# Optimization experiments

Hardware: AMD Instinct MI355X
Metric: run time of the kernel (lower is better)

## Reference

```python
import jax, jax.numpy as jnp
import numpy as np
import math

B, S, E, H, DK, DV = 2, 2048, 1024, 16, 64, 64
EPS = 1e-06


def setup_inputs() -> dict:
    key = jax.random.key(0)
    ks = jax.random.split(key, 11)
    s_in = 1.0 / math.sqrt(E)
    return {
        "query": jax.random.normal(ks[0], (B, S, E), jnp.float32),
        "key_in": jax.random.normal(ks[1], (B, S, E), jnp.float32),
        "value_in": jax.random.normal(ks[2], (B, S, E), jnp.float32),
        "residual_x": jax.random.normal(ks[3], (B, S, E), jnp.float32),
        # stacked per-head Linear params (torch Linear: y = x @ W.T + b); here W stored as [H, E, d]
        "Wq": jax.random.uniform(ks[4], (H, E, DK), jnp.float32, -s_in, s_in),
        "bq": jax.random.uniform(ks[5], (H, DK), jnp.float32, -s_in, s_in),
        "Wk": jax.random.uniform(ks[6], (H, E, DK), jnp.float32, -s_in, s_in),
        "bk": jax.random.uniform(ks[7], (H, DK), jnp.float32, -s_in, s_in),
        "Wv": jax.random.uniform(ks[8], (H, E, DV), jnp.float32, -s_in, s_in),
        "bv": jax.random.uniform(ks[9], (H, DV), jnp.float32, -s_in, s_in),
        "ln_scale": jnp.ones((E,), jnp.float32),
        "ln_shift": jnp.zeros((E,), jnp.float32),
    }


def reference(query, key_in, value_in, residual_x, Wq, bq, Wk, bk, Wv, bv, ln_scale, ln_shift):
    # batched per-head projections (replaces python loop over heads)
    q = jnp.einsum("bse,hed->bhsd", query, Wq) + bq[None, :, None, :]
    k = jnp.einsum("bse,hed->bhsd", key_in, Wk) + bk[None, :, None, :]
    v = jnp.einsum("bse,hed->bhsd", value_in, Wv) + bv[None, :, None, :]
    scores = jnp.einsum("bhsd,bhtd->bhst", q, k) / math.sqrt(DK)  # [B,H,S,S]
    causal = jnp.tril(jnp.ones((S, S), bool))  # mask strictly-upper triangle to -inf
    scores = jnp.where(causal[None, None], scores, -jnp.inf)
    attn = jax.nn.softmax(scores, axis=-1)
    out = jnp.einsum("bhst,bhtd->bhsd", attn, v)
    # concat heads along feature dim (head order = cat order)
    out = out.transpose(0, 2, 1, 3).reshape(B, S, H * DV)
    x = out + residual_x
    # custom LayerNorm: unbiased std, shift added into denominator
    mean = x.mean(-1, keepdims=True)
    std = jnp.sqrt(jnp.sum((x - mean) ** 2, axis=-1, keepdims=True) / (E - 1))
    div = std + EPS + ln_shift  # broadcasts [B,S,1]+[E] -> [B,S,E]
    return ln_scale * (x - mean) / div
```

## Files before the change

### kernel.cpp

```cpp
#include <hip/hip_runtime.h>
#include <hip/hip_bf16.h>

#define NB 2
#define NS 2048
#define NE 1024
#define NH 16
#define ND 64
#define MTOT (NB * NS)

typedef __attribute__((ext_vector_type(8))) short bf8_t;
typedef __attribute__((ext_vector_type(4))) short bf4_t;
typedef __attribute__((ext_vector_type(4))) float f32x4;

__device__ __forceinline__ short f2bf(float f) {
    union { float f; unsigned u; } v; v.f = f;
    return (short)((v.u + 0x7FFFu + ((v.u >> 16) & 1u)) >> 16);
}

#define GLOAD16(g, l) __builtin_amdgcn_global_load_lds( \
    (const __attribute__((address_space(1))) void*)(g), \
    (__attribute__((address_space(3))) void*)(l), 16, 0, 0)

__global__ __launch_bounds__(256) void conv_kernel(
    const float* __restrict__ src, short* __restrict__ out)
{
    const size_t nchunk = (size_t)MTOT * NE / 8;
    const size_t stride = (size_t)gridDim.x * 256;
    for (size_t i = (size_t)blockIdx.x * 256 + threadIdx.x; i < nchunk; i += stride) {
        size_t e = i * 8;
        float4 x0 = *(const float4*)(src + e);
        float4 x1 = *(const float4*)(src + e + 4);
        bf8_t o;
        o[0] = f2bf(x0.x); o[1] = f2bf(x0.y); o[2] = f2bf(x0.z); o[3] = f2bf(x0.w);
        o[4] = f2bf(x1.x); o[5] = f2bf(x1.y); o[6] = f2bf(x1.z); o[7] = f2bf(x1.w);
        *(bf8_t*)(out + e) = o;
    }
}

__global__ __launch_bounds__(256) void wt_kernel(
    const float* __restrict__ Wq, const float* __restrict__ Wk, const float* __restrict__ Wv,
    short* __restrict__ wt)
{
    const int p = blockIdx.x / NH, h = blockIdx.x % NH;
    const int e0 = blockIdx.y * 64;
    const float* W = (p == 0) ? Wq : (p == 1) ? Wk : Wv;
    const int t = threadIdx.x;
    const int er = t >> 2, dc = (t & 3) * 16;
    const float* src = W + ((size_t)h * NE + e0 + er) * ND + dc;
    short* dst = wt + (size_t)(p * NH + h) * ND * NE;
#pragma unroll
    for (int j = 0; j < 16; j += 4) {
        float4 x = *(const float4*)(src + j);
        dst[(size_t)(dc + j + 0) * NE + e0 + er] = f2bf(x.x);
        dst[(size_t)(dc + j + 1) * NE + e0 + er] = f2bf(x.y);
        dst[(size_t)(dc + j + 2) * NE + e0 + er] = f2bf(x.z);
        dst[(size_t)(dc + j + 3) * NE + e0 + er] = f2bf(x.w);
    }
}

__global__ __launch_bounds__(256) void proj_kernel(
    const short* __restrict__ A, const short* __restrict__ Bm,
    const float* __restrict__ bias_all, int p, short* __restrict__ outp)
{
    __shared__ __attribute__((aligned(16))) short As[128 * 32];
    __shared__ __attribute__((aligned(16))) short Bs[128 * 32];

    const int m0 = blockIdx.x * 128, n0 = blockIdx.y * 128;
    const int t = threadIdx.x, lane = t & 63, w = t >> 6;
    const int l15 = lane & 15, g = lane >> 4;
    const int wr = w >> 1, wc = w & 1;

    const int srow = t >> 2, scol = (t & 3) * 8;
    const short* ag = A + (size_t)(m0 + srow) * NE + scol;
    const short* bg = Bm + (size_t)(n0 + srow) * NE + scol;
    short* asl = As + t * 8;
    short* bsl = Bs + t * 8;

    f32x4 acc[4][4];
#pragma unroll
    for (int i = 0; i < 4; ++i)
#pragma unroll
        for (int j = 0; j < 4; ++j) acc[i][j] = (f32x4){0.f, 0.f, 0.f, 0.f};

    for (int k0 = 0; k0 < NE; k0 += 32) {
        __syncthreads();
        GLOAD16(ag + k0, asl);
        GLOAD16(ag + k0 + (size_t)64 * NE, asl + 2048);
        GLOAD16(bg + k0, bsl);
        GLOAD16(bg + k0 + (size_t)64 * NE, bsl + 2048);
        __syncthreads();
        bf8_t af[4], bfr[4];
#pragma unroll
        for (int mf = 0; mf < 4; ++mf)
            af[mf] = *(const bf8_t*)&As[(wr * 64 + mf * 16 + l15) * 32 + g * 8];
#pragma unroll
        for (int nf = 0; nf < 4; ++nf)
            bfr[nf] = *(const bf8_t*)&Bs[(wc * 64 + nf * 16 + l15) * 32 + g * 8];
#pragma unroll
        for (int mf = 0; mf < 4; ++mf)
#pragma unroll
            for (int nf = 0; nf < 4; ++nf)
                acc[mf][nf] = __builtin_amdgcn_mfma_f32_16x16x32_bf16(af[mf], bfr[nf], acc[mf][nf], 0, 0, 0);
    }

    const int h = (n0 + wc * 64) >> 6;
    const float* bias = bias_all + h * ND;

    if (p < 2) {
#pragma unroll
        for (int mf = 0; mf < 4; ++mf) {
            const int m = m0 + wr * 64 + mf * 16 + g * 4;
            const int bb = m >> 11, s = m & (NS - 1);
#pragma unroll
            for (int nf = 0; nf < 4; ++nf) {
                const int d = nf * 16 + l15;
                const float bi = bias[d];
                short* op = outp + (((size_t)bb * NH + h) * NS + s) * ND + d;
#pragma unroll
                for (int r = 0; r < 4; ++r)
                    op[(size_t)r * ND] = f2bf(acc[mf][nf][r] + bi);
            }
        }
    } else {
#pragma unroll
        for (int mf = 0; mf < 4; ++mf) {
            const int m = m0 + wr * 64 + mf * 16 + g * 4;
            const int bb = m >> 11, s = m & (NS - 1);
#pragma unroll
            for (int nf = 0; nf < 4; ++nf) {
                const int d = nf * 16 + l15;
                const float bi = bias[d];
                bf4_t pk;
#pragma unroll
                for (int r = 0; r < 4; ++r) pk[r] = f2bf(acc[mf][nf][r] + bi);
                *(bf4_t*)&outp[(((size_t)bb * NH + h) * ND + d) * NS + s] = pk;
            }
        }
    }
}

__global__ __launch_bounds__(256) void attn_kernel(
    const short* __restrict__ q_ws, const short* __restrict__ k_ws,
    const short* __restrict__ vT_ws, float* __restrict__ O)
{
    __shared__ __attribute__((aligned(16))) short Qs[64][72];
    __shared__ __attribute__((aligned(16))) short Ks[64][72];
    __shared__ __attribute__((aligned(16))) short Vt[64][72];
    __shared__ __attribute__((aligned(16))) short Ps[4][16][72];

    const int bh = blockIdx.x;
    const int qt = (int)gridDim.y - 1 - (int)blockIdx.y;
    const int b = bh >> 4, h = bh & 15;
    const int t = threadIdx.x, lane = t & 63, w = t >> 6;
    const int l15 = lane & 15, g = lane >> 4, g8 = g * 8;
    const size_t base = (size_t)bh * NS * ND;
    const int q0 = qt * 64;

    const int srow = t >> 2, sc = (t & 3) * 16;
    {
        const short* src = q_ws + base + (size_t)(q0 + srow) * ND + sc;
        *(bf8_t*)&Qs[srow][sc] = *(const bf8_t*)src;
        *(bf8_t*)&Qs[srow][sc + 8] = *(const bf8_t*)(src + 8);
    }

    f32x4 oacc[4];
#pragma unroll
    for (int i = 0; i < 4; ++i) oacc[i] = (f32x4){0.f, 0.f, 0.f, 0.f};
    float m_i[4], l_i[4];
#pragma unroll
    for (int r = 0; r < 4; ++r) { m_i[r] = -1e30f; l_i[r] = 0.f; }

    const int qrow_base = q0 + w * 16 + g * 4;

    for (int tt = 0; tt <= qt; ++tt) {
        const int t0 = tt * 64;
        __syncthreads();
        {
            const short* ksrc = k_ws + base + (size_t)(t0 + srow) * ND + sc;
            *(bf8_t*)&Ks[srow][sc] = *(const bf8_t*)ksrc;
            *(bf8_t*)&Ks[srow][sc + 8] = *(const bf8_t*)(ksrc + 8);
            const short* vsrc = vT_ws + base + (size_t)srow * NS + t0 + sc;
            *(bf8_t*)&Vt[srow][sc] = *(const bf8_t*)vsrc;
            *(bf8_t*)&Vt[srow][sc + 8] = *(const bf8_t*)(vsrc + 8);
        }
        __syncthreads();

        f32x4 sa[4];
#pragma unroll
        for (int i = 0; i < 4; ++i) sa[i] = (f32x4){0.f, 0.f, 0.f, 0.f};
#pragma unroll
        for (int ks = 0; ks < 2; ++ks) {
            bf8_t af = *(const bf8_t*)&Qs[w * 16 + l15][ks * 32 + g8];
#pragma unroll
            for (int nb = 0; nb < 4; ++nb) {
                bf8_t bf = *(const bf8_t*)&Ks[nb * 16 + l15][ks * 32 + g8];
                sa[nb] = __builtin_amdgcn_mfma_f32_16x16x32_bf16(af, bf, sa[nb], 0, 0, 0);
            }
        }

        const bool diag = (tt == qt);
        float mloc[4] = {-1e30f, -1e30f, -1e30f, -1e30f};
#pragma unroll
        for (int nb = 0; nb < 4; ++nb)
#pragma unroll
            for (int r = 0; r < 4; ++r) {
                float sv = sa[nb][r] * 0.125f;
                if (diag && (t0 + nb * 16 + l15 > qrow_base + r)) sv = -1e30f;
                sa[nb][r] = sv;
                mloc[r] = fmaxf(mloc[r], sv);
            }
#pragma unroll
        for (int off = 1; off < 16; off <<= 1)
#pragma unroll
            for (int r = 0; r < 4; ++r)
                mloc[r] = fmaxf(mloc[r], __shfl_xor(mloc[r], off));

        float alpha[4], rs[4];
#pragma unroll
        for (int r = 0; r < 4; ++r) {
            float mn = fmaxf(m_i[r], mloc[r]);
            alpha[r] = __expf(m_i[r] - mn);
            m_i[r] = mn;
            rs[r] = 0.f;
        }
#pragma unroll
        for (int nb = 0; nb < 4; ++nb)
#pragma unroll
            for (int r = 0; r < 4; ++r) {
                float pv = __expf(sa[nb][r] - m_i[r]);
                sa[nb][r] = pv;
                rs[r] += pv;
            }
#pragma unroll
        for (int off = 1; off < 16; off <<= 1)
#pragma unroll
            for (int r = 0; r < 4; ++r)
                rs[r] += __shfl_xor(rs[r], off);
#pragma unroll
        for (int r = 0; r < 4; ++r) l_i[r] = l_i[r] * alpha[r] + rs[r];
#pragma unroll
        for (int nb = 0; nb < 4; ++nb)
#pragma unroll
            for (int r = 0; r < 4; ++r) oacc[nb][r] *= alpha[r];

#pragma unroll
        for (int nb = 0; nb < 4; ++nb)
#pragma unroll
            for (int r = 0; r < 4; ++r)
                Ps[w][g * 4 + r][nb * 16 + l15] = f2bf(sa[nb][r]);

#pragma unroll
        for (int ks = 0; ks < 2; ++ks) {
            bf8_t pf = *(const bf8_t*)&Ps[w][l15][ks * 32 + g8];
#pragma unroll
            for (int nb = 0; nb < 4; ++nb) {
                bf8_t vf = *(const bf8_t*)&Vt[nb * 16 + l15][ks * 32 + g8];
                oacc[nb] = __builtin_amdgcn_mfma_f32_16x16x32_bf16(pf, vf, oacc[nb], 0, 0, 0);
            }
        }
    }

#pragma unroll
    for (int r = 0; r < 4; ++r) {
        float inv = 1.0f / l_i[r];
        int qg = qrow_base + r;
#pragma unroll
        for (int nb = 0; nb < 4; ++nb)
            O[((size_t)b * NS + qg) * NE + h * ND + nb * 16 + l15] = oacc[nb][r] * inv;
    }
}

__global__ __launch_bounds__(256) void ln_kernel(
    const float* __restrict__ Oin, const float* __restrict__ resid,
    const float* __restrict__ ln_scale, const float* __restrict__ ln_shift,
    float* __restrict__ out)
{
    __shared__ float red[8];
    const int row = blockIdx.x, t = threadIdx.x;
    const size_t basei = (size_t)row * NE + t * 4;
    float4 x = *(const float4*)(Oin + basei);
    float4 rr = *(const float4*)(resid + basei);
    x.x += rr.x; x.y += rr.y; x.z += rr.z; x.w += rr.w;
    float ps = x.x + x.y + x.z + x.w;
#pragma unroll
    for (int off = 32; off; off >>= 1) ps += __shfl_xor(ps, off);
    if ((t & 63) == 0) red[t >> 6] = ps;
    __syncthreads();
    const float mean = (red[0] + red[1] + red[2] + red[3]) * (1.0f / NE);
    const float dx0 = x.x - mean, dx1 = x.y - mean, dx2 = x.z - mean, dx3 = x.w - mean;
    float ss = dx0 * dx0 + dx1 * dx1 + dx2 * dx2 + dx3 * dx3;
#pragma unroll
    for (int off = 32; off; off >>= 1) ss += __shfl_xor(ss, off);
    if ((t & 63) == 0) red[4 + (t >> 6)] = ss;
    __syncthreads();
    const float stdv = sqrtf((red[4] + red[5] + red[6] + red[7]) * (1.0f / (NE - 1)));
    float4 sc = *(const float4*)(ln_scale + t * 4);
    float4 sh = *(const float4*)(ln_shift + t * 4);
    float4 o;
    o.x = sc.x * dx0 / (stdv + 1e-6f + sh.x);
    o.y = sc.y * dx1 / (stdv + 1e-6f + sh.y);
    o.z = sc.z * dx2 / (stdv + 1e-6f + sh.z);
    o.w = sc.w * dx3 / (stdv + 1e-6f + sh.w);
    *(float4*)(out + basei) = o;
}

extern "C" void kernel_launch(void* const* d_in, const int* in_sizes, int n_in,
                              void* d_out, int out_size, void* d_ws, size_t ws_size,
                              hipStream_t stream) {
    (void)in_sizes; (void)n_in; (void)out_size; (void)ws_size;
    const float* query    = (const float*)d_in[0];
    const float* key_in   = (const float*)d_in[1];
    const float* value_in = (const float*)d_in[2];
    const float* resid    = (const float*)d_in[3];
    const float* Wq = (const float*)d_in[4];
    const float* bq = (const float*)d_in[5];
    const float* Wk = (const float*)d_in[6];
    const float* bk = (const float*)d_in[7];
    const float* Wv = (const float*)d_in[8];
    const float* bv = (const float*)d_in[9];
    const float* ln_scale = (const float*)d_in[10];
    const float* ln_shift = (const float*)d_in[11];
    float* out = (float*)d_out;

    char* ws = (char*)d_ws;
    short* wt_ws = (short*)ws;
    short* in_bf = (short*)(ws + (6u << 20));
    short* q_ws  = (short*)(ws + (14u << 20));
    short* k_ws  = (short*)(ws + (22u << 20));
    short* vT_ws = (short*)(ws + (30u << 20));
    float* O_ws  = (float*)ws;

    wt_kernel<<<dim3(3 * NH, NE / 64), 256, 0, stream>>>(Wq, Wk, Wv, wt_ws);

    const float* ins[3]   = {query, key_in, value_in};
    const float* biases[3] = {bq, bk, bv};
    short* outs[3] = {q_ws, k_ws, vT_ws};
    for (int p = 0; p < 3; ++p) {
        conv_kernel<<<1024, 256, 0, stream>>>(ins[p], in_bf);
        proj_kernel<<<dim3(MTOT / 128, NE / 128), 256, 0, stream>>>(
            in_bf, wt_ws + (size_t)p * NE * NE, biases[p], p, outs[p]);
    }

    attn_kernel<<<dim3(NB * NH, NS / 64), 256, 0, stream>>>(q_ws, k_ws, vT_ws, O_ws);
    ln_kernel<<<dim3(NB * NS), 256, 0, stream>>>(O_ws, resid, ln_scale, ln_shift, out);
}
```

Before: 297.2 us.

## Rewrite attention as per-wave 32x32 MFMA flash loop with register-resident K/V

The attention kernel is restructured so each wave independently handles 32 query rows using 32x32x16 MFMAs. K and V fragments load straight from global memory into registers, which removes the LDS staging and block-level barriers. Softmax moves to the exp2 domain: the 1/sqrt(d)*log2(e) factor is folded into the Q projection, and rescaling is lazy, running only when the running max grows by more than a threshold. The Q and K projections are batched into one launch with a z-grid dimension, which cuts launch overhead. Output is transposed through LDS to give coalesced stores. The risks are more redundant global K/V traffic per wave and extra register pressure.

```diff
diff --git a/kernel.cpp b/kernel.cpp
--- a/kernel.cpp
+++ b/kernel.cpp
@@ -8,13 +8,28 @@
 #define ND 64
 #define MTOT (NB * NS)
 
+#define QSCALE 0.18033688011112042f
+
 typedef __attribute__((ext_vector_type(8))) short bf8_t;
 typedef __attribute__((ext_vector_type(4))) short bf4_t;
 typedef __attribute__((ext_vector_type(4))) float f32x4;
+typedef __attribute__((ext_vector_type(16))) float f32x16;
 
 __device__ __forceinline__ short f2bf(float f) {
     union { float f; unsigned u; } v; v.f = f;
     return (short)((v.u + 0x7FFFu + ((v.u >> 16) & 1u)) >> 16);
+}
+
+__device__ __forceinline__ unsigned cvtpk(float lo, float hi) {
+    unsigned r;
+    asm("v_cvt_pk_bf16_f32 %0, %1, %2" : "=v"(r) : "v"(lo), "v"(hi));
+    return r;
+}
+
+__device__ __forceinline__ bf8_t mk4(unsigned a, unsigned b, unsigned c, unsigned d) {
+    union { unsigned u[4]; bf8_t v; } t;
+    t.u[0] = a; t.u[1] = b; t.u[2] = c; t.u[3] = d;
+    return t.v;
 }
 
 #define GLOAD16(g, l) __builtin_amdgcn_global_load_lds( \
@@ -59,11 +74,19 @@
 }
 
 __global__ __launch_bounds__(256) void proj_kernel(
-    const short* __restrict__ A, const short* __restrict__ Bm,
-    const float* __restrict__ bias_all, int p, short* __restrict__ outp)
+    const short* __restrict__ in_bf, const short* __restrict__ wt,
+    const float* __restrict__ bq, const float* __restrict__ bk, const float* __restrict__ bv,
+    short* __restrict__ q_ws, short* __restrict__ k_ws, short* __restrict__ vT_ws,
+    int pbase)
 {
     __shared__ __attribute__((aligned(16))) short As[128 * 32];
     __shared__ __attribute__((aligned(16))) short Bs[128 * 32];
+
+    const int z = blockIdx.z, p = pbase + z;
+    const short* A = in_bf + (size_t)z * MTOT * NE;
+    const short* Bm = wt + (size_t)p * NE * NE;
+    const float* bias_all = (p == 0) ? bq : (p == 1) ? bk : bv;
+    const float oscale = (p == 0) ? QSCALE : 1.0f;
 
     const int m0 = blockIdx.x * 128, n0 = blockIdx.y * 128;
     const int t = threadIdx.x, lane = t & 63, w = t >> 6;
@@ -107,6 +130,7 @@
     const float* bias = bias_all + h * ND;
 
     if (p < 2) {
+        short* outp = (p == 0) ? q_ws : k_ws;
 #pragma unroll
         for (int mf = 0; mf < 4; ++mf) {
             const int m = m0 + wr * 64 + mf * 16 + g * 4;
@@ -118,7 +142,7 @@
                 short* op = outp + (((size_t)bb * NH + h) * NS + s) * ND + d;
 #pragma unroll
                 for (int r = 0; r < 4; ++r)
-                    op[(size_t)r * ND] = f2bf(acc[mf][nf][r] + bi);
+                    op[(size_t)r * ND] = f2bf((acc[mf][nf][r] + bi) * oscale);
             }
         }
     } else {
@@ -133,140 +157,143 @@
                 bf4_t pk;
 #pragma unroll
                 for (int r = 0; r < 4; ++r) pk[r] = f2bf(acc[mf][nf][r] + bi);
-                *(bf4_t*)&outp[(((size_t)bb * NH + h) * ND + d) * NS + s] = pk;
+                *(bf4_t*)&vT_ws[(((size_t)bb * NH + h) * ND + d) * NS + s] = pk;
             }
         }
     }
 }
 
-__global__ __launch_bounds__(256) void attn_kernel(
+__global__ __launch_bounds__(256, 2) void attn_kernel(
     const short* __restrict__ q_ws, const short* __restrict__ k_ws,
     const short* __restrict__ vT_ws, float* __restrict__ O)
 {
-    __shared__ __attribute__((aligned(16))) short Qs[64][72];
-    __shared__ __attribute__((aligned(16))) short Ks[64][72];
-    __shared__ __attribute__((aligned(16))) short Vt[64][72];
-    __shared__ __attribute__((aligned(16))) short Ps[4][16][72];
-
-    const int bh = blockIdx.x;
-    const int qt = (int)gridDim.y - 1 - (int)blockIdx.y;
+    __shared__ float oT[4][32][65];
+    const int t = threadIdx.x, lane = t & 63, w = t >> 6;
+    const int g = (int)blockIdx.x * 4 + w;
+    const int jq = 63 - (g >> 5);
+    const int bh = g & 31;
     const int b = bh >> 4, h = bh & 15;
-    const int t = threadIdx.x, lane = t & 63, w = t >> 6;
-    const int l15 = lane & 15, g = lane >> 4, g8 = g * 8;
+    const int q0w = jq * 32;
+    const int nt = (jq >> 1) + 1;
+    const int l31 = lane & 31, hi = lane >> 5;
     const size_t base = (size_t)bh * NS * ND;
-    const int q0 = qt * 64;
-
-    const int srow = t >> 2, sc = (t & 3) * 16;
+
+    bf8_t Qf[4];
     {
-        const short* src = q_ws + base + (size_t)(q0 + srow) * ND + sc;
-        *(bf8_t*)&Qs[srow][sc] = *(const bf8_t*)src;
-        *(bf8_t*)&Qs[srow][sc + 8] = *(const bf8_t*)(src + 8);
-    }
-
-    f32x4 oacc[4];
-#pragma unroll
-    for (int i = 0; i < 4; ++i) oacc[i] = (f32x4){0.f, 0.f, 0.f, 0.f};
-    float m_i[4], l_i[4];
-#pragma unroll
-    for (int r = 0; r < 4; ++r) { m_i[r] = -1e30f; l_i[r] = 0.f; }
-
-    const int qrow_base = q0 + w * 16 + g * 4;
-
-    for (int tt = 0; tt <= qt; ++tt) {
+        const short* qsrc = q_ws + base + (size_t)(q0w + l31) * ND + hi * 8;
+#pragma unroll
+        for (int s = 0; s < 4; ++s) Qf[s] = *(const bf8_t*)(qsrc + s * 16);
+    }
+
+    f32x16 Oa[2];
+#pragma unroll
+    for (int rb = 0; rb < 2; ++rb)
+#pragma unroll
+        for (int r = 0; r < 16; ++r) Oa[rb][r] = 0.f;
+    float m_i = -1e30f, l_i = 0.f;
+    const int qg = q0w + l31;
+
+    for (int tt = 0; tt < nt; ++tt) {
         const int t0 = tt * 64;
-        __syncthreads();
-        {
-            const short* ksrc = k_ws + base + (size_t)(t0 + srow) * ND + sc;
-            *(bf8_t*)&Ks[srow][sc] = *(const bf8_t*)ksrc;
-            *(bf8_t*)&Ks[srow][sc + 8] = *(const bf8_t*)(ksrc + 8);
-            const short* vsrc = vT_ws + base + (size_t)srow * NS + t0 + sc;
-            *(bf8_t*)&Vt[srow][sc] = *(const bf8_t*)vsrc;
-            *(bf8_t*)&Vt[srow][sc + 8] = *(const bf8_t*)(vsrc + 8);
-        }
-        __syncthreads();
-
-        f32x4 sa[4];
-#pragma unroll
-        for (int i = 0; i < 4; ++i) sa[i] = (f32x4){0.f, 0.f, 0.f, 0.f};
-#pragma unroll
-        for (int ks = 0; ks < 2; ++ks) {
-            bf8_t af = *(const bf8_t*)&Qs[w * 16 + l15][ks * 32 + g8];
-#pragma unroll
-            for (int nb = 0; nb < 4; ++nb) {
-                bf8_t bf = *(const bf8_t*)&Ks[nb * 16 + l15][ks * 32 + g8];
-                sa[nb] = __builtin_amdgcn_mfma_f32_16x16x32_bf16(af, bf, sa[nb], 0, 0, 0);
+
+        bf8_t Kf[2][4];
+#pragma unroll
+        for (int c = 0; c < 2; ++c) {
+            const short* kp = k_ws + base + (size_t)(t0 + c * 32 + l31) * ND + hi * 8;
+#pragma unroll
+            for (int s = 0; s < 4; ++s) Kf[c][s] = *(const bf8_t*)(kp + s * 16);
+        }
+        bf8_t Vf[4][2];
+#pragma unroll
+        for (int rb = 0; rb < 2; ++rb) {
+            const short* vp = vT_ws + base + (size_t)(rb * 32 + l31) * NS + t0 + hi * 8;
+#pragma unroll
+            for (int cs = 0; cs < 4; ++cs) Vf[cs][rb] = *(const bf8_t*)(vp + cs * 16);
+        }
+
+        f32x16 Sv[2];
+#pragma unroll
+        for (int c = 0; c < 2; ++c) {
+#pragma unroll
+            for (int r = 0; r < 16; ++r) Sv[c][r] = 0.f;
+#pragma unroll
+            for (int s = 0; s < 4; ++s)
+                Sv[c] = __builtin_amdgcn_mfma_f32_32x32x16_bf16(Kf[c][s], Qf[s], Sv[c], 0, 0, 0);
+        }
+
+        if (tt == nt - 1) {
+#pragma unroll
+            for (int c = 0; c < 2; ++c)
+#pragma unroll
+                for (int r = 0; r < 16; ++r) {
+                    const int kvg = t0 + c * 32 + (r & 3) + 8 * (r >> 2) + 4 * hi;
+                    if (kvg > qg) Sv[c][r] = -1e30f;
+                }
+        }
+
+        float mloc = Sv[0][0];
+#pragma unroll
+        for (int r = 1; r < 16; ++r) mloc = fmaxf(mloc, Sv[0][r]);
+#pragma unroll
+        for (int r = 0; r < 16; ++r) mloc = fmaxf(mloc, Sv[1][r]);
+        mloc = fmaxf(mloc, __shfl_xor(mloc, 32));
+
+        if (__any(mloc > m_i + 11.0f)) {
+            const float mn = fmaxf(m_i, mloc);
+            const float al = exp2f(m_i - mn);
+            m_i = mn;
+            l_i *= al;
+#pragma unroll
+            for (int rb = 0; rb < 2; ++rb)
+#pragma unroll
+                for (int r = 0; r < 16; ++r) Oa[rb][r] *= al;
+        }
+
+        float rs = 0.f;
+        bf8_t Pf[2][2];
+#pragma unroll
+        for (int c = 0; c < 2; ++c) {
+#pragma unroll
+            for (int r = 0; r < 16; ++r) {
+                const float pv = exp2f(Sv[c][r] - m_i);
+                Sv[c][r] = pv;
+                rs += pv;
             }
-        }
-
-        const bool diag = (tt == qt);
-        float mloc[4] = {-1e30f, -1e30f, -1e30f, -1e30f};
-#pragma unroll
-        for (int nb = 0; nb < 4; ++nb)
-#pragma unroll
-            for (int r = 0; r < 4; ++r) {
-                float sv = sa[nb][r] * 0.125f;
-                if (diag && (t0 + nb * 16 + l15 > qrow_base + r)) sv = -1e30f;
-                sa[nb][r] = sv;
-                mloc[r] = fmaxf(mloc[r], sv);
-            }
-#pragma unroll
-        for (int off = 1; off < 16; off <<= 1)
-#pragma unroll
-            for (int r = 0; r < 4; ++r)
-                mloc[r] = fmaxf(mloc[r], __shfl_xor(mloc[r], off));
-
-        float alpha[4], rs[4];
-#pragma unroll
-        for (int r = 0; r < 4; ++r) {
-            float mn = fmaxf(m_i[r], mloc[r]);
-            alpha[r] = __expf(m_i[r] - mn);
-            m_i[r] = mn;
-            rs[r] = 0.f;
-        }
-#pragma unroll
-        for (int nb = 0; nb < 4; ++nb)
-#pragma unroll
-            for (int r = 0; r < 4; ++r) {
-                float pv = __expf(sa[nb][r] - m_i[r]);
-                sa[nb][r] = pv;
-                rs[r] += pv;
-            }
-#pragma unroll
-        for (int off = 1; off < 16; off <<= 1)
-#pragma unroll
-            for (int r = 0; r < 4; ++r)
-                rs[r] += __shfl_xor(rs[r], off);
-#pragma unroll
-        for (int r = 0; r < 4; ++r) l_i[r] = l_i[r] * alpha[r] + rs[r];
-#pragma unroll
-        for (int nb = 0; nb < 4; ++nb)
-#pragma unroll
-            for (int r = 0; r < 4; ++r) oacc[nb][r] *= alpha[r];
-
-#pragma unroll
-        for (int nb = 0; nb < 4; ++nb)
-#pragma unroll
-            for (int r = 0; r < 4; ++r)
-                Ps[w][g * 4 + r][nb * 16 + l15] = f2bf(sa[nb][r]);
-
-#pragma unroll
-        for (int ks = 0; ks < 2; ++ks) {
-            bf8_t pf = *(const bf8_t*)&Ps[w][l15][ks * 32 + g8];
-#pragma unroll
-            for (int nb = 0; nb < 4; ++nb) {
-                bf8_t vf = *(const bf8_t*)&Vt[nb * 16 + l15][ks * 32 + g8];
-                oacc[nb] = __builtin_amdgcn_mfma_f32_16x16x32_bf16(pf, vf, oacc[nb], 0, 0, 0);
-            }
-        }
-    }
-
-#pragma unroll
-    for (int r = 0; r < 4; ++r) {
-        float inv = 1.0f / l_i[r];
-        int qg = qrow_base + r;
-#pragma unroll
-        for (int nb = 0; nb < 4; ++nb)
-            O[((size_t)b * NS + qg) * NE + h * ND + nb * 16 + l15] = oacc[nb][r] * inv;
+            unsigned wv[8], xv[8];
+#pragma unroll
+            for (int i = 0; i < 8; ++i) wv[i] = cvtpk(Sv[c][2 * i], Sv[c][2 * i + 1]);
+#pragma unroll
+            for (int i = 0; i < 8; ++i) xv[i] = __shfl_xor(wv[i], 32);
+            Pf[c][0] = hi ? mk4(xv[2], xv[3], wv[2], wv[3]) : mk4(wv[0], wv[1], xv[0], xv[1]);
+            Pf[c][1] = hi ? mk4(xv[6], xv[7], wv[6], wv[7]) : mk4(wv[4], wv[5], xv[4], xv[5]);
+        }
+        rs += __shfl_xor(rs, 32);
+        l_i += rs;
+
+#pragma unroll
+        for (int cs = 0; cs < 4; ++cs)
+#pragma unroll
+            for (int rb = 0; rb < 2; ++rb)
+                Oa[rb] = __builtin_amdgcn_mfma_f32_32x32x16_bf16(Vf[cs][rb], Pf[cs >> 1][cs & 1], Oa[rb], 0, 0, 0);
+    }
+
+    const float inv = 1.0f / l_i;
+#pragma unroll
+    for (int rb = 0; rb < 2; ++rb)
+#pragma unroll
+        for (int r = 0; r < 16; ++r)
+            oT[w][l31][rb * 32 + (r & 3) + 8 * (r >> 2) + 4 * hi] = Oa[rb][r] * inv;
+
+    asm volatile("s_waitcnt lgkmcnt(0)" ::: "memory");
+
+#pragma unroll
+    for (int p4 = 0; p4 < 4; ++p4) {
+        const int qr = p4 * 8 + (lane >> 3), d8 = (lane & 7) * 8;
+        const float4 a0 = *(const float4*)&oT[w][qr][d8];
+        const float4 a1 = *(const float4*)&oT[w][qr][d8 + 4];
+        float* op = O + ((size_t)b * NS + q0w + qr) * NE + h * 64 + d8;
+        *(float4*)op = a0;
+        *(float4*)(op + 4) = a1;
     }
 }
 
@@ -325,22 +352,25 @@
     char* ws = (char*)d_ws;
     short* wt_ws = (short*)ws;
     short* in_bf = (short*)(ws + (6u << 20));
-    short* q_ws  = (short*)(ws + (14u << 20));
-    short* k_ws  = (short*)(ws + (22u << 20));
-    short* vT_ws = (short*)(ws + (30u << 20));
+    short* q_ws  = (short*)(ws + (22u << 20));
+    short* k_ws  = (short*)(ws + (30u << 20));
+    short* vT_ws = (short*)(ws + (38u << 20));
     float* O_ws  = (float*)ws;
 
+    short* slot0 = in_bf;
+    short* slot1 = in_bf + (size_t)MTOT * NE;
+
     wt_kernel<<<dim3(3 * NH, NE / 64), 256, 0, stream>>>(Wq, Wk, Wv, wt_ws);
 
-    const float* ins[3]   = {query, key_in, value_in};
-    const float* biases[3] = {bq, bk, bv};
-    short* outs[3] = {q_ws, k_ws, vT_ws};
-    for (int p = 0; p < 3; ++p) {
-        conv_kernel<<<1024, 256, 0, stream>>>(ins[p], in_bf);
-        proj_kernel<<<dim3(MTOT / 128, NE / 128), 256, 0, stream>>>(
-            in_bf, wt_ws + (size_t)p * NE * NE, biases[p], p, outs[p]);
-    }
-
-    attn_kernel<<<dim3(NB * NH, NS / 64), 256, 0, stream>>>(q_ws, k_ws, vT_ws, O_ws);
+    conv_kernel<<<1024, 256, 0, stream>>>(query, slot0);
+    conv_kernel<<<1024, 256, 0, stream>>>(key_in, slot1);
+    proj_kernel<<<dim3(MTOT / 128, NE / 128, 2), 256, 0, stream>>>(
+        in_bf, wt_ws, bq, bk, bv, q_ws, k_ws, vT_ws, 0);
+
+    conv_kernel<<<1024, 256, 0, stream>>>(value_in, slot0);
+    proj_kernel<<<dim3(MTOT / 128, NE / 128, 1), 256, 0, stream>>>(
+        in_bf, wt_ws, bq, bk, bv, q_ws, k_ws, vT_ws, 2);
+
+    attn_kernel<<<512, 256, 0, stream>>>(q_ws, k_ws, vT_ws, O_ws);
     ln_kernel<<<dim3(NB * NS), 256, 0, stream>>>(O_ws, resid, ln_scale, ln_shift, out);
 }
```

New measurement: 285.0 us. -4.1%, faster.
